# Optimization experiments

Hardware: AMD Instinct MI355X
Metric: run time of the kernel (lower is better)

Reference implementation:

```python
import jax, jax.numpy as jnp
import numpy as np

N_NODES = 100000
N_EDGES = 6400000


def setup_inputs() -> dict:
    key = jax.random.key(0)
    k1, k2, k3, k4 = jax.random.split(key, 4)
    x = jax.random.normal(k1, (N_NODES, 9), dtype=jnp.float32)
    edge_index = jax.random.randint(k2, (2, N_EDGES), 0, N_NODES, dtype=jnp.int64)
    W1 = jax.random.normal(k3, (9, 16), dtype=jnp.float32) * (1.0 / np.sqrt(9))
    b1 = jnp.zeros((16,), dtype=jnp.float32)
    W2 = jax.random.normal(k4, (16, 1), dtype=jnp.float32) * (1.0 / np.sqrt(16))
    b2 = jnp.zeros((1,), dtype=jnp.float32)
    return {"x": x, "edge_index": edge_index, "W1": W1, "b1": b1, "W2": W2, "b2": b2}


def _gcn_norm(edge_index, num_nodes):
    # Add self-loops (GCNConv default) and compute symmetric normalization.
    loops = jnp.arange(num_nodes, dtype=edge_index.dtype)
    row = jnp.concatenate([edge_index[0], loops])  # source
    col = jnp.concatenate([edge_index[1], loops])  # destination
    deg = jax.ops.segment_sum(jnp.ones_like(col, dtype=jnp.float32), col,
                              num_segments=num_nodes)
    dinv = jnp.where(deg > 0, jax.lax.rsqrt(deg), 0.0)
    norm = dinv[row] * dinv[col]  # [E + N]
    return row, col, norm


def _gcn_conv(h, row, col, norm, W, b, num_nodes):
    h = h @ W                                    # [N, F_out] tiny GEMM
    msg = h[row] * norm[:, None]                 # gather + per-edge scale
    out = jax.ops.segment_sum(msg, col, num_segments=num_nodes)  # scatter-add
    return out + b


def reference(x, edge_index, W1, b1, W2, b2):
    num_nodes = x.shape[0]
    row, col, norm = _gcn_norm(edge_index, num_nodes)
    h = _gcn_conv(x.astype(jnp.float32), row, col, norm, W1, b1, num_nodes)
    h = jax.nn.relu(h)
    # F.dropout(training=self.training) is identity in eval mode
    h = _gcn_conv(h, row, col, norm, W2, b2, num_nodes)
    return jax.nn.relu(h)
```

## Files before the change

kernel.cpp:

```cpp
#include <hip/hip_runtime.h>
#include <hip/hip_fp16.h>

#define NN 100000
#define NE 6400000
#define NCO 1024
#define BSZC 98
#define NB2 512
#define CHUNK2 12500
#define TOTB (NCO * NB2)
#define SC1 2048
#define NCH (TOTB / SC1)
#define CAPS 7424
#define MAXIT 15
#define CAPB 16


__global__ __launch_bounds__(512) void histA(const int* __restrict__ col, int* __restrict__ X) {
    __shared__ int h[NCO];
    for (int i = threadIdx.x; i < NCO; i += 512) h[i] = 0;
    __syncthreads();
    const int4* c4 = (const int4*)(col + blockIdx.x * CHUNK2);
    for (int i = threadIdx.x; i < CHUNK2 / 4; i += 512) {
        int4 v = c4[i];
        atomicAdd(&h[(unsigned)v.x / BSZC], 1);
        atomicAdd(&h[(unsigned)v.y / BSZC], 1);
        atomicAdd(&h[(unsigned)v.z / BSZC], 1);
        atomicAdd(&h[(unsigned)v.w / BSZC], 1);
    }
    __syncthreads();
    int* o = X + blockIdx.x * NCO;
    for (int i = threadIdx.x; i < NCO; i += 512) o[i] = h[i];
}

__global__ __launch_bounds__(512) void scan1(int* __restrict__ X, int* __restrict__ ctot) {
    __shared__ int buf[SC1];
    __shared__ int ts[512];
    int base = blockIdx.x * SC1;
    for (int j = threadIdx.x; j < SC1; j += 512) {
        int idx = base + j;
        int k = idx >> 9, b = idx & 511;
        buf[j] = X[(b << 10) | k];
    }
    __syncthreads();
    int j0 = threadIdx.x * 4;
    int a0 = buf[j0], a1 = buf[j0 + 1], a2 = buf[j0 + 2], a3 = buf[j0 + 3];
    int s = a0 + a1 + a2 + a3;
    ts[threadIdx.x] = s;
    __syncthreads();
    for (int off = 1; off < 512; off <<= 1) {
        int u = (threadIdx.x >= off) ? ts[threadIdx.x - off] : 0;
        __syncthreads();
        ts[threadIdx.x] += u;
        __syncthreads();
    }
    int e0 = ts[threadIdx.x] - s;
    int ev[4] = {e0, e0 + a0, e0 + a0 + a1, e0 + a0 + a1 + a2};
#pragma unroll
    for (int t = 0; t < 4; ++t) {
        int idx = base + j0 + t;
        int k = idx >> 9, b = idx & 511;
        X[(b << 10) | k] = ev[t];
    }
    if (threadIdx.x == 511) ctot[blockIdx.x] = ts[511];
}

__global__ void scan2(const int* __restrict__ ctot, int* __restrict__ cbase) {
    __shared__ int ts[1024];
    int t = threadIdx.x;
    int orig = (t < NCH) ? ctot[t] : 0;
    ts[t] = orig;
    __syncthreads();
    for (int off = 1; off < 1024; off <<= 1) {
        int u = (t >= off) ? ts[t - off] : 0;
        __syncthreads();
        ts[t] += u;
        __syncthreads();
    }
    if (t < NCH) cbase[t] = ts[t] - orig;
}

__global__ __launch_bounds__(256) void scan3(int* __restrict__ X, const int* __restrict__ cbase) {
    int m = blockIdx.x * 256 + threadIdx.x;
    if (m >= TOTB) return;
    int hb = m >> 10;
    int c = m & 1023;
    int idx = (c << 9) | hb;
    X[m] += cbase[idx >> 11];
}

__global__ __launch_bounds__(512) void passB1(const int* __restrict__ row, const int* __restrict__ col,
                                              const int* __restrict__ X, int* __restrict__ eb) {
    __shared__ int buf[NCO][CAPB];
    __shared__ int cnt[NCO];
    __shared__ int sbase[NCO];
    int hb = ((blockIdx.x & 7) << 6) | (blockIdx.x >> 3);
    const int* st = X + (hb << 10);
    for (int i = threadIdx.x; i < NCO; i += 512) { cnt[i] = 0; sbase[i] = st[i]; }
    __syncthreads();
    const int4* c4 = (const int4*)(col + hb * CHUNK2);
    const int4* r4 = (const int4*)(row + hb * CHUNK2);
    for (int i = threadIdx.x; i < CHUNK2 / 4; i += 512) {
        int4 cc = c4[i];
        int4 rr = r4[i];
        int cq[4] = {cc.x, cc.y, cc.z, cc.w};
        int rq[4] = {rr.x, rr.y, rr.z, rr.w};
#pragma unroll
        for (int q = 0; q < 4; ++q) {
            int k = (unsigned)cq[q] / BSZC;
            int word = rq[q] | ((cq[q] - k * BSZC) << 17);
            int pos = atomicAdd(&cnt[k], 1);
            if (pos < CAPB) buf[k][pos] = word;
            else            eb[sbase[k] + pos] = word;
        }
    }
    __syncthreads();
    int w = threadIdx.x >> 6, lane = threadIdx.x & 63;
    int sub = lane >> 4, l16 = lane & 15;
    for (int j = 0; j < 32; ++j) {
        int k = w * 128 + j * 4 + sub;
        int m = cnt[k]; if (m > CAPB) m = CAPB;
        if (l16 < m) eb[sbase[k] + l16] = buf[k][l16];
    }
}

__global__ __launch_bounds__(512) void passG(int* __restrict__ eb, const int* __restrict__ X,
                                             const float* __restrict__ x, const float* __restrict__ W1,
                                             float* __restrict__ dinv, int* __restrict__ rs,
                                             unsigned short* __restrict__ g1h) {
    __shared__ float sW[144];
    __shared__ int seg2[CAPS];
    __shared__ int cnt8[8][128];
    __shared__ int wb[8][128];
    __shared__ int binpf[128];
    __shared__ int tot[128];
    int c = blockIdx.x;
    int s = X[c];
    int e = (c + 1 < NCO) ? X[c + 1] : NE;
    int n = e - s; if (n > CAPS) n = CAPS;
    for (int i = threadIdx.x; i < 144; i += 512) sW[i] = W1[i];
    if (c == 0 && threadIdx.x == 0) rs[NN] = NE;
    int w = threadIdx.x >> 6, lane = threadIdx.x & 63;
    unsigned long long lowm = (1ull << lane) - 1ull;
    int q0 = (n + 7) >> 3;
    int ws_ = w * q0;
    int we_ = ws_ + q0; if (we_ > n) we_ = n;
    int niter = (we_ > ws_) ? ((we_ - ws_ + 63) >> 6) : 0;
    int arr[MAXIT];
    int c0 = 0, c1 = 0;
#pragma unroll
    for (int it = 0; it < MAXIT; ++it) {
        if (it < niter) {
            int i = ws_ + it * 64 + lane;
            bool val = (i < we_);
            int p = val ? eb[s + i] : 0;
            int key = (p >> 17) & 127;
            unsigned long long b0 = __ballot(val && (key & 1));
            unsigned long long b1 = __ballot(val && (key & 2));
            unsigned long long b2 = __ballot(val && (key & 4));
            unsigned long long b3 = __ballot(val && (key & 8));
            unsigned long long b4 = __ballot(val && (key & 16));
            unsigned long long b5 = __ballot(val && (key & 32));
            unsigned long long b6 = __ballot(val && (key & 64));
            unsigned long long bv = __ballot(val);
            unsigned long long own = ((key & 1) ? b0 : ~b0)
                                   & ((key & 2) ? b1 : ~b1)
                                   & ((key & 4) ? b2 : ~b2)
                                   & ((key & 8) ? b3 : ~b3)
                                   & ((key & 16) ? b4 : ~b4)
                                   & ((key & 32) ? b5 : ~b5)
                                   & ((key & 64) ? b6 : ~b6) & bv;
            int rank = __popcll(own & lowm);
            int p0 = __shfl(c0, key & 63);
            int p1 = __shfl(c1, key & 63);
            int prior = (key & 64) ? p1 : p0;
            arr[it] = p | ((prior + rank) << 24);
            unsigned long long mlow = ((lane & 1) ? b0 : ~b0)
                                    & ((lane & 2) ? b1 : ~b1)
                                    & ((lane & 4) ? b2 : ~b2)
                                    & ((lane & 8) ? b3 : ~b3)
                                    & ((lane & 16) ? b4 : ~b4)
                                    & ((lane & 32) ? b5 : ~b5) & bv;
            c0 += __popcll(mlow & ~b6);
            c1 += __popcll(mlow & b6);
        }
    }
    cnt8[w][lane] = c0;
    cnt8[w][lane + 64] = c1;
    __syncthreads();
    if (threadIdx.x < 64) {
        int l = threadIdx.x;
        int t0 = 0, t1 = 0;
#pragma unroll
        for (int q = 0; q < 8; ++q) { t0 += cnt8[q][l * 2]; t1 += cnt8[q][l * 2 + 1]; }
        int ps = t0 + t1;
        int pf = ps;
#pragma unroll
        for (int d = 1; d < 64; d <<= 1) {
            int u = __shfl(pf, l - d);
            if (l >= d) pf += u;
        }
        int excl = pf - ps;
        binpf[l * 2] = excl;
        binpf[l * 2 + 1] = excl + t0;
        tot[l * 2] = t0; tot[l * 2 + 1] = t1;
    }
    __syncthreads();
    if (threadIdx.x < 128) {
        int bin = threadIdx.x;
        int acc = binpf[bin];
#pragma unroll
        for (int q = 0; q < 8; ++q) { wb[q][bin] = acc; acc += cnt8[q][bin]; }
        if (bin < BSZC) {
            int node = c * BSZC + bin;
            if (node < NN) {
                rs[node] = s + binpf[bin];
                dinv[node] = rsqrtf((float)tot[bin] + 1.f);
            }
        }
    }
    __syncthreads();
#pragma unroll
    for (int it = 0; it < MAXIT; ++it) {
        if (it < niter) {
            int i = ws_ + it * 64 + lane;
            if (i < we_) {
                int pw = arr[it];
                int key = (pw >> 17) & 127;
                int lr = (unsigned)pw >> 24;
                seg2[wb[w][key] + lr] = pw & 0x1FFFF;
            }
        }
    }
    __syncthreads();
    for (int i = threadIdx.x; i < n; i += 512) eb[s + i] = seg2[i];
    int nd = threadIdx.x >> 2, fq = threadIdx.x & 3;
    if (nd < BSZC) {
        int node = c * BSZC + nd;
        if (node < NN) {
            float di = rsqrtf((float)tot[nd] + 1.f);
            float xr[9];
#pragma unroll
            for (int q = 0; q < 9; ++q) xr[q] = x[node * 9 + q];
            float a[4];
#pragma unroll
            for (int j = 0; j < 4; ++j) {
                int ff = fq * 4 + j;
                float acc = 0.f;
#pragma unroll
                for (int q = 0; q < 9; ++q) acc = fmaf(xr[q], sW[q * 16 + ff], acc);
                a[j] = acc * di;
            }
            __half2 h0 = __floats2half2_rn(a[0], a[1]);
            __half2 h1 = __floats2half2_rn(a[2], a[3]);
            uint2 stv;
            stv.x = *(unsigned int*)&h0; stv.y = *(unsigned int*)&h1;
            *(uint2*)((char*)g1h + (size_t)node * 32 + fq * 8) = stv;
        }
    }
}

__global__ __launch_bounds__(256) void passE(const int* __restrict__ eb, const int* __restrict__ rs,
                                             const unsigned short* __restrict__ g1h,
                                             const float* __restrict__ dinv,
                                             const float* __restrict__ b1, const float* __restrict__ W2,
                                             float* __restrict__ gg) {
    __shared__ float sb1[16], sW2[16];
    if (threadIdx.x < 16) { sb1[threadIdx.x] = b1[threadIdx.x]; sW2[threadIdx.x] = W2[threadIdx.x]; }
    __syncthreads();
    int w = threadIdx.x >> 6, lane = threadIdx.x & 63;
    int k = blockIdx.x * 4 + w;
    if (k >= 6250) return;
    int g = lane >> 2, fq = lane & 3;
    const char* gb = (const char*)g1h;
    for (int nd = 0; nd < 16; ++nd) {
        int node = k * 16 + nd;
        int rsv = rs[node], rev = rs[node + 1];
        int base = rsv & ~3;
        int t4 = (rev - base + 3) >> 2;
        const int4* ebv = (const int4*)(eb + base);
        float4 acc = make_float4(0.f, 0.f, 0.f, 0.f);
        for (int it = g; it < t4; it += 16) {
            int4 pk = ebv[it];
            int ib = base + it * 4;
            int pq[4] = {pk.x, pk.y, pk.z, pk.w};
#pragma unroll
            for (int q = 0; q < 4; ++q) {
                int idx = ib + q;
                bool v = (idx >= rsv) && (idx < rev);
                int r = v ? (pq[q] & 0x1FFFF) : 0;
                uint2 hv = *(const uint2*)(gb + (size_t)r * 32 + fq * 8);
                __half2 h0 = *(__half2*)&hv.x, h1 = *(__half2*)&hv.y;
                float2 f0 = __half22float2(h0), f1 = __half22float2(h1);
                if (v) {
                    acc.x += f0.x; acc.y += f0.y; acc.z += f1.x; acc.w += f1.y;
                }
            }
        }
#pragma unroll
        for (int d = 4; d < 64; d <<= 1) {
            acc.x += __shfl_xor(acc.x, d);
            acc.y += __shfl_xor(acc.y, d);
            acc.z += __shfl_xor(acc.z, d);
            acc.w += __shfl_xor(acc.w, d);
        }
        float di = dinv[node];
        uint2 sv = *(const uint2*)(gb + (size_t)node * 32 + fq * 8);
        __half2 s0 = *(__half2*)&sv.x, s1 = *(__half2*)&sv.y;
        float2 gs0 = __half22float2(s0), gs1 = __half22float2(s1);
        int f0 = fq * 4;
        float v0 = fmaxf(di * (acc.x + gs0.x) + sb1[f0 + 0], 0.f);
        float v1 = fmaxf(di * (acc.y + gs0.y) + sb1[f0 + 1], 0.f);
        float v2 = fmaxf(di * (acc.z + gs1.x) + sb1[f0 + 2], 0.f);
        float v3 = fmaxf(di * (acc.w + gs1.y) + sb1[f0 + 3], 0.f);
        float part = v0 * sW2[f0] + v1 * sW2[f0 + 1] + v2 * sW2[f0 + 2] + v3 * sW2[f0 + 3];
        part += __shfl_xor(part, 1);
        part += __shfl_xor(part, 2);
        if (lane == 0) gg[node] = di * part;
    }
}

__global__ __launch_bounds__(256) void passF(const int* __restrict__ eb, const int* __restrict__ rs,
                                             const float* __restrict__ gg, const float* __restrict__ dinv,
                                             const float* __restrict__ b2, float* __restrict__ out) {
    int w = threadIdx.x >> 6, lane = threadIdx.x & 63;
    int k = blockIdx.x * 4 + w;
    if (k >= 6250) return;
    float b = b2[0];
    int l = lane & 31;
    int half = lane >> 5;
    for (int nd0 = 0; nd0 < 16; nd0 += 2) {
        int node = k * 16 + nd0 + half;
        int rsv = rs[node], rev = rs[node + 1];
        float a = 0.f;
        for (int i = rsv + l; i < rev; i += 32) a += gg[eb[i] & 0x1FFFF];
#pragma unroll
        for (int d = 1; d < 32; d <<= 1) a += __shfl_xor(a, d);
        if (l == 0) out[node] = fmaxf(dinv[node] * (a + gg[node]) + b, 0.f);
    }
}


__global__ void fb_deg(const int* __restrict__ col, float* __restrict__ deg, int E) {
    int stride = gridDim.x * blockDim.x;
    for (int i = blockIdx.x * blockDim.x + threadIdx.x; i < E; i += stride)
        atomicAdd(&deg[col[i]], 1.0f);
}
__global__ void fb_dinv(float* __restrict__ d, int N) {
    int i = blockIdx.x * blockDim.x + threadIdx.x;
    if (i < N) d[i] = rsqrtf(d[i] + 1.0f);
}
__global__ void fb_h1p(const float* __restrict__ x, const float* __restrict__ W1, float* __restrict__ h1p, int N) {
    __shared__ float sW[144];
    if (threadIdx.x < 144) sW[threadIdx.x] = W1[threadIdx.x];
    __syncthreads();
    int i = blockIdx.x * blockDim.x + threadIdx.x;
    if (i >= N) return;
    float xi[9];
#pragma unroll
    for (int q = 0; q < 9; ++q) xi[q] = x[i * 9 + q];
#pragma unroll
    for (int ff = 0; ff < 16; ++ff) {
        float a = 0.f;
#pragma unroll
        for (int q = 0; q < 9; ++q) a = fmaf(xi[q], sW[q * 16 + ff], a);
        h1p[i * 16 + ff] = a;
    }
}
__global__ void fb_sc1(const int* __restrict__ row, const int* __restrict__ col, const float* __restrict__ dinv,
                       const float* __restrict__ h1p, float* __restrict__ agg1, long total) {
    long stride = (long)gridDim.x * blockDim.x;
    for (long t = (long)blockIdx.x * blockDim.x + threadIdx.x; t < total; t += stride) {
        int e = (int)(t >> 4), ff = (int)(t & 15);
        int r = row[e], c = col[e];
        atomicAdd(&agg1[c * 16 + ff], h1p[r * 16 + ff] * dinv[r] * dinv[c]);
    }
}
__global__ void fb_fin1(const float* __restrict__ agg1, const float* __restrict__ h1p, const float* __restrict__ dinv,
                        const float* __restrict__ b1, const float* __restrict__ W2, float* __restrict__ h2p, int N) {
    __shared__ float sW2[16], sb1[16];
    if (threadIdx.x < 16) { sW2[threadIdx.x] = W2[threadIdx.x]; sb1[threadIdx.x] = b1[threadIdx.x]; }
    __syncthreads();
    int i = blockIdx.x * blockDim.x + threadIdx.x;
    if (i >= N) return;
    float di = dinv[i], self = di * di, a = 0.f;
#pragma unroll
    for (int ff = 0; ff < 16; ++ff) {
        float v = agg1[i * 16 + ff] + h1p[i * 16 + ff] * self + sb1[ff];
        a = fmaf(fmaxf(v, 0.f), sW2[ff], a);
    }
    h2p[i] = a;
}
__global__ void fb_sc2(const int* __restrict__ row, const int* __restrict__ col, const float* __restrict__ dinv,
                       const float* __restrict__ h2p, float* __restrict__ out, int E) {
    int stride = gridDim.x * blockDim.x;
    for (int e = blockIdx.x * blockDim.x + threadIdx.x; e < E; e += stride) {
        int r = row[e], c = col[e];
        atomicAdd(&out[c], h2p[r] * dinv[r] * dinv[c]);
    }
}
__global__ void fb_fin2(float* __restrict__ out, const float* __restrict__ h2p, const float* __restrict__ dinv,
                        const float* __restrict__ b2, int N) {
    int i = blockIdx.x * blockDim.x + threadIdx.x;
    if (i < N) {
        float di = dinv[i];
        out[i] = fmaxf(out[i] + h2p[i] * di * di + b2[0], 0.f);
    }
}


extern "C" void kernel_launch(void* const* d_in, const int* in_sizes, int n_in,
                              void* d_out, int out_size, void* d_ws, size_t ws_size,
                              hipStream_t stream) {
    const float* x  = (const float*)d_in[0];
    const int*   ei = (const int*)d_in[1];
    const float* W1 = (const float*)d_in[2];
    const float* b1 = (const float*)d_in[3];
    const float* W2 = (const float*)d_in[4];
    const float* b2 = (const float*)d_in[5];
    float* out = (float*)d_out;
    const int* row = ei;
    const int* col = ei + NE;
    char* ws = (char*)d_ws;

    constexpr size_t OFF_EB  = 0;
    constexpr size_t OFF_X   = 25600000;
    constexpr size_t OFF_CT  = OFF_X + 2097152;
    constexpr size_t OFF_CB  = OFF_CT + 4096;
    constexpr size_t OFF_DI  = OFF_CB + 4096;
    constexpr size_t OFF_RS  = OFF_DI + 400000;
    constexpr size_t OFF_GG  = OFF_RS + 400128;
    constexpr size_t OFF_G1H = OFF_GG + 400000;
    constexpr size_t WS_NEED = OFF_G1H + 3200000 + 4194304;

    if (ws_size >= WS_NEED) {
        int*   eb    = (int*)(ws + OFF_EB);
        int*   X     = (int*)(ws + OFF_X);
        int*   ctot  = (int*)(ws + OFF_CT);
        int*   cbase = (int*)(ws + OFF_CB);
        float* dinv  = (float*)(ws + OFF_DI);
        int*   rs    = (int*)(ws + OFF_RS);
        float* gg    = (float*)(ws + OFF_GG);
        unsigned short* g1h = (unsigned short*)(ws + OFF_G1H);

        histA<<<NB2, 512, 0, stream>>>(col, X);
        scan1<<<NCH, 512, 0, stream>>>(X, ctot);
        scan2<<<1, 1024, 0, stream>>>(ctot, cbase);
        scan3<<<(TOTB + 255) / 256, 256, 0, stream>>>(X, cbase);
        passB1<<<NB2, 512, 0, stream>>>(row, col, X, eb);
        passG<<<NCO, 512, 0, stream>>>(eb, X, x, W1, dinv, rs, g1h);
        int gridK = (6250 + 3) / 4;
        passE<<<gridK, 256, 0, stream>>>(eb, rs, g1h, dinv, b1, W2, gg);
        passF<<<gridK, 256, 0, stream>>>(eb, rs, gg, dinv, b2, out);
    } else {
        float* dinv = (float*)(ws);
        float* h1p  = (float*)(ws + 524288);
        float* agg1 = (float*)(ws + 6924288);
        float* h2p  = (float*)(ws + 13324288);
        hipMemsetAsync(dinv, 0, NN * sizeof(float), stream);
        hipMemsetAsync(agg1, 0, NN * 16 * sizeof(float), stream);
        hipMemsetAsync(out, 0, NN * sizeof(float), stream);
        const int B = 256;
        int gridN = (NN + B - 1) / B;
        fb_deg<<<4096, B, 0, stream>>>(col, dinv, NE);
        fb_dinv<<<gridN, B, 0, stream>>>(dinv, NN);
        fb_h1p<<<gridN, B, 0, stream>>>(x, W1, h1p, NN);
        fb_sc1<<<8192, B, 0, stream>>>(row, col, dinv, h1p, agg1, (long)NE * 16);
        fb_fin1<<<gridN, B, 0, stream>>>(agg1, h1p, dinv, b1, W2, h2p, NN);
        fb_sc2<<<4096, B, 0, stream>>>(row, col, dinv, h2p, out, NE);
        fb_fin2<<<gridN, B, 0, stream>>>(out, h2p, dinv, b2, NN);
    }
}
```

Baseline: 164.4 us.

## Process four nodes per wavefront in gather passes and stage sort keys in LDS

The two CSR gather kernels (passE and passF) now split each 64-lane wavefront into four 16-lane groups, each handling one node, instead of one or two nodes per wave. With average degree around 64, this keeps more lanes busy and shortens the shuffle reductions. In passG, the unrolled per-thread register array used for the in-block counting sort is replaced by an LDS staging buffer. That removes the MAXIT cap and register pressure but costs extra shared memory, which may reduce occupancy.

```diff
diff --git a/kernel.cpp b/kernel.cpp
--- a/kernel.cpp
+++ b/kernel.cpp
@@ -11,7 +11,6 @@
 #define SC1 2048
 #define NCH (TOTB / SC1)
 #define CAPS 7424
-#define MAXIT 15
 #define CAPB 16
 
 
@@ -128,6 +127,7 @@
                                              float* __restrict__ dinv, int* __restrict__ rs,
                                              unsigned short* __restrict__ g1h) {
     __shared__ float sW[144];
+    __shared__ int stage[CAPS];
     __shared__ int seg2[CAPS];
     __shared__ int cnt8[8][128];
     __shared__ int wb[8][128];
@@ -144,45 +144,40 @@
     int q0 = (n + 7) >> 3;
     int ws_ = w * q0;
     int we_ = ws_ + q0; if (we_ > n) we_ = n;
-    int niter = (we_ > ws_) ? ((we_ - ws_ + 63) >> 6) : 0;
-    int arr[MAXIT];
     int c0 = 0, c1 = 0;
-#pragma unroll
-    for (int it = 0; it < MAXIT; ++it) {
-        if (it < niter) {
-            int i = ws_ + it * 64 + lane;
-            bool val = (i < we_);
-            int p = val ? eb[s + i] : 0;
-            int key = (p >> 17) & 127;
-            unsigned long long b0 = __ballot(val && (key & 1));
-            unsigned long long b1 = __ballot(val && (key & 2));
-            unsigned long long b2 = __ballot(val && (key & 4));
-            unsigned long long b3 = __ballot(val && (key & 8));
-            unsigned long long b4 = __ballot(val && (key & 16));
-            unsigned long long b5 = __ballot(val && (key & 32));
-            unsigned long long b6 = __ballot(val && (key & 64));
-            unsigned long long bv = __ballot(val);
-            unsigned long long own = ((key & 1) ? b0 : ~b0)
-                                   & ((key & 2) ? b1 : ~b1)
-                                   & ((key & 4) ? b2 : ~b2)
-                                   & ((key & 8) ? b3 : ~b3)
-                                   & ((key & 16) ? b4 : ~b4)
-                                   & ((key & 32) ? b5 : ~b5)
-                                   & ((key & 64) ? b6 : ~b6) & bv;
-            int rank = __popcll(own & lowm);
-            int p0 = __shfl(c0, key & 63);
-            int p1 = __shfl(c1, key & 63);
-            int prior = (key & 64) ? p1 : p0;
-            arr[it] = p | ((prior + rank) << 24);
-            unsigned long long mlow = ((lane & 1) ? b0 : ~b0)
-                                    & ((lane & 2) ? b1 : ~b1)
-                                    & ((lane & 4) ? b2 : ~b2)
-                                    & ((lane & 8) ? b3 : ~b3)
-                                    & ((lane & 16) ? b4 : ~b4)
-                                    & ((lane & 32) ? b5 : ~b5) & bv;
-            c0 += __popcll(mlow & ~b6);
-            c1 += __popcll(mlow & b6);
-        }
+    for (int i0 = ws_; i0 < we_; i0 += 64) {
+        int i = i0 + lane;
+        bool val = (i < we_);
+        int p = val ? eb[s + i] : 0;
+        int key = (p >> 17) & 127;
+        unsigned long long b0 = __ballot(val && (key & 1));
+        unsigned long long b1 = __ballot(val && (key & 2));
+        unsigned long long b2 = __ballot(val && (key & 4));
+        unsigned long long b3 = __ballot(val && (key & 8));
+        unsigned long long b4 = __ballot(val && (key & 16));
+        unsigned long long b5 = __ballot(val && (key & 32));
+        unsigned long long b6 = __ballot(val && (key & 64));
+        unsigned long long bv = __ballot(val);
+        unsigned long long own = ((key & 1) ? b0 : ~b0)
+                               & ((key & 2) ? b1 : ~b1)
+                               & ((key & 4) ? b2 : ~b2)
+                               & ((key & 8) ? b3 : ~b3)
+                               & ((key & 16) ? b4 : ~b4)
+                               & ((key & 32) ? b5 : ~b5)
+                               & ((key & 64) ? b6 : ~b6) & bv;
+        int rank = __popcll(own & lowm);
+        int p0 = __shfl(c0, key & 63);
+        int p1 = __shfl(c1, key & 63);
+        int prior = (key & 64) ? p1 : p0;
+        if (val) stage[i] = p | ((prior + rank) << 24);
+        unsigned long long mlow = ((lane & 1) ? b0 : ~b0)
+                                & ((lane & 2) ? b1 : ~b1)
+                                & ((lane & 4) ? b2 : ~b2)
+                                & ((lane & 8) ? b3 : ~b3)
+                                & ((lane & 16) ? b4 : ~b4)
+                                & ((lane & 32) ? b5 : ~b5) & bv;
+        c0 += __popcll(mlow & ~b6);
+        c1 += __popcll(mlow & b6);
     }
     cnt8[w][lane] = c0;
     cnt8[w][lane + 64] = c1;
@@ -219,16 +214,13 @@
         }
     }
     __syncthreads();
-#pragma unroll
-    for (int it = 0; it < MAXIT; ++it) {
-        if (it < niter) {
-            int i = ws_ + it * 64 + lane;
-            if (i < we_) {
-                int pw = arr[it];
-                int key = (pw >> 17) & 127;
-                int lr = (unsigned)pw >> 24;
-                seg2[wb[w][key] + lr] = pw & 0x1FFFF;
-            }
+    for (int i0 = ws_; i0 < we_; i0 += 64) {
+        int i = i0 + lane;
+        if (i < we_) {
+            int pw = stage[i];
+            int key = (pw >> 17) & 127;
+            int lr = (unsigned)pw >> 24;
+            seg2[wb[w][key] + lr] = pw & 0x1FFFF;
         }
     }
     __syncthreads();
@@ -270,16 +262,19 @@
     int w = threadIdx.x >> 6, lane = threadIdx.x & 63;
     int k = blockIdx.x * 4 + w;
     if (k >= 6250) return;
-    int g = lane >> 2, fq = lane & 3;
+    int sub = lane >> 4;
+    int l16 = lane & 15;
+    int g = l16 >> 2;
+    int fq = l16 & 3;
     const char* gb = (const char*)g1h;
-    for (int nd = 0; nd < 16; ++nd) {
-        int node = k * 16 + nd;
+    for (int nd0 = 0; nd0 < 16; nd0 += 4) {
+        int node = k * 16 + nd0 + sub;
         int rsv = rs[node], rev = rs[node + 1];
         int base = rsv & ~3;
         int t4 = (rev - base + 3) >> 2;
         const int4* ebv = (const int4*)(eb + base);
         float4 acc = make_float4(0.f, 0.f, 0.f, 0.f);
-        for (int it = g; it < t4; it += 16) {
+        for (int it = g; it < t4; it += 4) {
             int4 pk = ebv[it];
             int ib = base + it * 4;
             int pq[4] = {pk.x, pk.y, pk.z, pk.w};
@@ -297,7 +292,7 @@
             }
         }
 #pragma unroll
-        for (int d = 4; d < 64; d <<= 1) {
+        for (int d = 4; d < 16; d <<= 1) {
             acc.x += __shfl_xor(acc.x, d);
             acc.y += __shfl_xor(acc.y, d);
             acc.z += __shfl_xor(acc.z, d);
@@ -315,7 +310,7 @@
         float part = v0 * sW2[f0] + v1 * sW2[f0 + 1] + v2 * sW2[f0 + 2] + v3 * sW2[f0 + 3];
         part += __shfl_xor(part, 1);
         part += __shfl_xor(part, 2);
-        if (lane == 0) gg[node] = di * part;
+        if (l16 == 0) gg[node] = di * part;
     }
 }
 
@@ -326,16 +321,15 @@
     int k = blockIdx.x * 4 + w;
     if (k >= 6250) return;
     float b = b2[0];
-    int l = lane & 31;
-    int half = lane >> 5;
-    for (int nd0 = 0; nd0 < 16; nd0 += 2) {
-        int node = k * 16 + nd0 + half;
+    int sub = lane >> 4, l16 = lane & 15;
+    for (int nd0 = 0; nd0 < 16; nd0 += 4) {
+        int node = k * 16 + nd0 + sub;
         int rsv = rs[node], rev = rs[node + 1];
         float a = 0.f;
-        for (int i = rsv + l; i < rev; i += 32) a += gg[eb[i] & 0x1FFFF];
-#pragma unroll
-        for (int d = 1; d < 32; d <<= 1) a += __shfl_xor(a, d);
-        if (l == 0) out[node] = fmaxf(dinv[node] * (a + gg[node]) + b, 0.f);
+        for (int i = rsv + l16; i < rev; i += 16) a += gg[eb[i] & 0x1FFFF];
+#pragma unroll
+        for (int d = 1; d < 16; d <<= 1) a += __shfl_xor(a, d);
+        if (l16 == 0) out[node] = fmaxf(dinv[node] * (a + gg[node]) + b, 0.f);
     }
 }
 
```

Measured after the change: 159.8 us (median of 2 runs). 1.03x faster.
